# Performance work log

Measured on AMD Instinct MI355X. Metric: run time of the kernel, lower is better.

Reference implementation:

```python
import jax, jax.numpy as jnp
import numpy as np

N = 32768; NS = 16; C_MAIN = 128; C_MOD = 128; C_IN = 16; SHARE = 8
EPS = 1e-5; CHUNK = 1024
C_OUT = C_MAIN + C_MOD  # out_main = in_main + in_mod
C_W = C_IN // SHARE     # attention-weight channels = 2


def _bn(x, g, b, m, v):
    # BatchNorm1d in eval mode, per last-dim channel
    return (x - m) / jnp.sqrt(v + EPS) * g + b


def _knn(p, k):
    # exact kNN (self included, distance 0), chunked to bound memory
    def f(q):  # q: (CHUNK, 3)
        d = jnp.sum((q[:, None, :] - p[None, :, :]) ** 2, axis=-1)  # (CHUNK, N)
        return jax.lax.top_k(-d, k)[1]
    return jax.lax.map(f, p.reshape(-1, CHUNK, 3)).reshape(-1, k)


def setup_inputs() -> dict:
    key = jax.random.key(0)
    ks = iter(jax.random.split(key, 24))
    rn = lambda shape, s=0.1: jax.random.normal(next(ks), shape, jnp.float32) * s
    inp = {}
    inp["x_main"] = jax.random.normal(next(ks), (N, C_MAIN), jnp.float32)
    inp["x_mod"] = jax.random.normal(next(ks), (N, C_MOD), jnp.float32)
    inp["xyz"] = jax.random.uniform(next(ks), (N, 3), dtype=jnp.float32)
    inp["W_ein"] = rn((C_OUT, C_IN)); inp["b_ein"] = rn((C_IN,))
    inp["W_eout"] = rn((C_IN, C_OUT)); inp["b_eout"] = rn((C_OUT,))
    inp["Wq"] = rn((C_IN, C_IN)); inp["bq"] = rn((C_IN,))
    inp["Wk"] = rn((C_IN, C_IN)); inp["bk"] = rn((C_IN,))
    inp["Wv"] = rn((C_IN, C_IN)); inp["bv"] = rn((C_IN,))
    inp["Wp1"] = rn((3, 3)); inp["bp1"] = rn((3,))
    inp["Wp2"] = rn((3, C_IN)); inp["bp2"] = rn((C_IN,))
    inp["Wl1"] = rn((C_IN, C_W)); inp["bl1"] = rn((C_W,))
    inp["Wl2"] = rn((C_W, C_W)); inp["bl2"] = rn((C_W,))
    for name, c in (("bn_p", 3), ("bn_w1", C_IN), ("bn_w2", C_W)):
        inp[name + "_g"] = jnp.ones(c, jnp.float32)
        inp[name + "_b"] = jnp.zeros(c, jnp.float32)
        inp[name + "_m"] = jnp.zeros(c, jnp.float32)
        inp[name + "_v"] = jnp.ones(c, jnp.float32)
    return inp


def _forward(x_main, x_mod, xyz, W_ein, b_ein, W_eout, b_eout, Wq, bq, Wk, bk, Wv, bv,
             Wp1, bp1, Wp2, bp2, Wl1, bl1, Wl2, bl2,
             bn_p_g, bn_p_b, bn_p_m, bn_p_v,
             bn_w1_g, bn_w1_b, bn_w1_m, bn_w1_v,
             bn_w2_g, bn_w2_b, bn_w2_m, bn_w2_v, idx):
    x_fused = jnp.concatenate([x_main, x_mod], axis=-1)   # (N, 256)
    x_res = x_fused
    h = x_fused @ W_ein + b_ein                           # E_in: (N, 16)
    # PointTransformerLayer (local vector self-attention over NS neighbors)
    xq = h @ Wq + bq
    xk = h @ Wk + bk
    xv = h @ Wv + bv
    p_r = xyz[idx] - xyz[:, None, :]                      # relative coords (N, NS, 3)
    g_k = xk[idx]                                         # grouped keys   (N, NS, 16)
    g_v = xv[idx]                                         # grouped values (N, NS, 16)
    # linear_p: Linear(3,3) -> BN -> ReLU -> Linear(3, C_IN)
    t = jax.nn.relu(_bn(p_r @ Wp1 + bp1, bn_p_g, bn_p_b, bn_p_m, bn_p_v))
    p_e = t @ Wp2 + bp2                                   # (N, NS, 16)
    # out_planes//mid_planes == 1, so the .view(...).sum(2) on p_e is identity
    w = g_k - xq[:, None, :] + p_e
    # linear_w: BN -> ReLU -> Linear(16,2) -> BN -> ReLU -> Linear(2,2)
    w = jax.nn.relu(_bn(w, bn_w1_g, bn_w1_b, bn_w1_m, bn_w1_v))
    w = w @ Wl1 + bl1
    w = jax.nn.relu(_bn(w, bn_w2_g, bn_w2_b, bn_w2_m, bn_w2_v))
    w = w @ Wl2 + bl2                                     # (N, NS, 2)
    w = jax.nn.softmax(w, axis=1)                         # softmax over neighbors
    agg = ((g_v + p_e).reshape(N, NS, SHARE, C_W) * w[:, :, None, :]).sum(1).reshape(N, C_IN)
    return agg @ W_eout + b_eout + x_res                  # E_out + residual


def reference(x_main, x_mod, xyz, W_ein, b_ein, W_eout, b_eout, Wq, bq, Wk, bk, Wv, bv,
              Wp1, bp1, Wp2, bp2, Wl1, bl1, Wl2, bl2,
              bn_p_g, bn_p_b, bn_p_m, bn_p_v,
              bn_w1_g, bn_w1_b, bn_w1_m, bn_w1_v,
              bn_w2_g, bn_w2_b, bn_w2_m, bn_w2_v):
    idx = _knn(xyz, NS)
    return _forward(x_main, x_mod, xyz, W_ein, b_ein, W_eout, b_eout, Wq, bq, Wk, bk, Wv, bv,
                    Wp1, bp1, Wp2, bp2, Wl1, bl1, Wl2, bl2,
                    bn_p_g, bn_p_b, bn_p_m, bn_p_v,
                    bn_w1_g, bn_w1_b, bn_w1_m, bn_w1_v,
                    bn_w2_g, bn_w2_b, bn_w2_m, bn_w2_v, idx)
```

## Files before the change

### kernel.cpp

```cpp
#include <hip/hip_runtime.h>
#include <cstdint>

#define NPTS 32768
#define K 16
#define G 16
#define NCELL (G*G*G)

typedef unsigned short u16;
typedef unsigned int u32;

__device__ __forceinline__ float bf(u16 v) { return __uint_as_float(((u32)v) << 16); }
__device__ __forceinline__ void unp(u32 u, float& a, float& b) {
    a = __uint_as_float(u << 16);
    b = __uint_as_float(u & 0xffff0000u);
}
__device__ __forceinline__ u32 f2b(float f) {
    u32 x = __float_as_uint(f);
    return (x + 0x7fffu + ((x >> 16) & 1u)) >> 16;
}
__device__ __forceinline__ float ldw(const void* p, int j, bool isb) {
    return isb ? bf(((const u16*)p)[j]) : ((const float*)p)[j];
}
__device__ __forceinline__ void ld8(const void* p, size_t i, int cb, bool isb, float xs[8]) {
    if (isb) {
        const uint4* r = (const uint4*)((const u16*)p + i * 128);
        const uint4 u = r[cb];
        unp(u.x, xs[0], xs[1]); unp(u.y, xs[2], xs[3]);
        unp(u.z, xs[4], xs[5]); unp(u.w, xs[6], xs[7]);
    } else {
        const float4* r = (const float4*)((const float*)p + i * 128);
        const float4 a = r[2 * cb], b = r[2 * cb + 1];
        xs[0] = a.x; xs[1] = a.y; xs[2] = a.z; xs[3] = a.w;
        xs[4] = b.x; xs[5] = b.y; xs[6] = b.z; xs[7] = b.w;
    }
}
__device__ __forceinline__ int cellco(float x) {
    int c = (int)(x * (float)G);
    return c < 0 ? 0 : (c > G - 1 ? G - 1 : c);
}

__global__ __launch_bounds__(128) void k_feats(
    const void* __restrict__ xm, const void* __restrict__ xd, const void* __restrict__ xyz,
    const void* __restrict__ Wein, const void* __restrict__ bein,
    const void* __restrict__ Wq, const void* __restrict__ bq,
    const void* __restrict__ Wk, const void* __restrict__ bk,
    const void* __restrict__ Wv, const void* __restrict__ bv,
    const u32* __restrict__ sigp,
    float* __restrict__ oq, float* __restrict__ ok, float* __restrict__ ov,
    float4* __restrict__ xyzf, int* __restrict__ cellCnt)
{
    const bool isb = (*sigp == 0x3F803F80u);
    __shared__ float sW[4096];
    __shared__ float sM[768];
    __shared__ float sB[64];
    const int t = threadIdx.x;
    if (blockIdx.x < 32) cellCnt[blockIdx.x * 128 + t] = 0;
    for (int u = t; u < 4096; u += 128) sW[u] = ldw(Wein, u, isb);
    for (int u = t; u < 256; u += 128) {
        sM[u] = ldw(Wq, u, isb); sM[256 + u] = ldw(Wk, u, isb); sM[512 + u] = ldw(Wv, u, isb);
    }
    if (t < 64) {
        const void* bsrc = (t < 16) ? bein : (t < 32) ? bq : (t < 48) ? bk : bv;
        sB[t] = ldw(bsrc, t & 15, isb);
    }
    __syncthreads();
    const int i = blockIdx.x * 128 + t;
    float h[16];
#pragma unroll
    for (int j = 0; j < 16; ++j) h[j] = sB[j];
#pragma unroll 2
    for (int cb = 0; cb < 32; ++cb) {
        float xs[8];
        ld8((cb < 16) ? xm : xd, (size_t)i, cb & 15, isb, xs);
        const int c0 = cb * 8;
#pragma unroll
        for (int u = 0; u < 8; ++u) {
            const float x = xs[u];
            const float* w = &sW[(c0 + u) * 16];
#pragma unroll
            for (int j = 0; j < 16; ++j) h[j] = fmaf(x, w[j], h[j]);
        }
    }
    float* outs[3] = { oq, ok, ov };
#pragma unroll
    for (int m3 = 0; m3 < 3; ++m3) {
        float acc[16];
#pragma unroll
        for (int j = 0; j < 16; ++j) acc[j] = sB[16 + m3 * 16 + j];
        const float* wm = &sM[m3 * 256];
#pragma unroll
        for (int m = 0; m < 16; ++m) {
            const float hm = h[m];
#pragma unroll
            for (int j = 0; j < 16; ++j) acc[j] = fmaf(hm, wm[m * 16 + j], acc[j]);
        }
        float* o = outs[m3] + (size_t)i * 16;
#pragma unroll
        for (int j = 0; j < 16; ++j) o[j] = acc[j];
    }
    if (isb) {
        const u16* z = (const u16*)xyz;
        xyzf[i] = make_float4(bf(z[i * 3]), bf(z[i * 3 + 1]), bf(z[i * 3 + 2]), 0.f);
    } else {
        const float* z = (const float*)xyz;
        xyzf[i] = make_float4(z[i * 3], z[i * 3 + 1], z[i * 3 + 2], 0.f);
    }
}

__global__ __launch_bounds__(256) void k_cell(const float4* __restrict__ xyzf,
    int* __restrict__ cellCnt, int* __restrict__ ptCell, int* __restrict__ ptRank)
{
    const int i = blockIdx.x * 256 + threadIdx.x;
    const float4 p = xyzf[i];
    const int c = (cellco(p.z) * G + cellco(p.y)) * G + cellco(p.x);
    ptCell[i] = c;
    ptRank[i] = atomicAdd(&cellCnt[c], 1);
}

__global__ __launch_bounds__(1024) void k_scan(const int* __restrict__ cnt, int* __restrict__ starts)
{
    __shared__ int part[1024];
    const int t = threadIdx.x;
    const int c0 = cnt[4 * t], c1 = cnt[4 * t + 1], c2 = cnt[4 * t + 2], c3 = cnt[4 * t + 3];
    const int s = c0 + c1 + c2 + c3;
    part[t] = s;
    __syncthreads();
    for (int off = 1; off < 1024; off <<= 1) {
        const int u = (t >= off) ? part[t - off] : 0;
        __syncthreads();
        part[t] += u;
        __syncthreads();
    }
    const int excl = part[t] - s;
    starts[4 * t] = excl;
    starts[4 * t + 1] = excl + c0;
    starts[4 * t + 2] = excl + c0 + c1;
    starts[4 * t + 3] = excl + c0 + c1 + c2;
    if (t == 1023) starts[NCELL] = part[1023];
}

__global__ __launch_bounds__(256) void k_scatter(const float4* __restrict__ xyzf,
    const int* __restrict__ ptCell, const int* __restrict__ ptRank,
    const int* __restrict__ starts, float4* __restrict__ sorted)
{
    const int i = blockIdx.x * 256 + threadIdx.x;
    float4 p = xyzf[i];
    p.w = __int_as_float(i);
    sorted[starts[ptCell[i]] + ptRank[i]] = p;
}

__device__ __forceinline__ bool lexlt(float d1, int i1, float d2, int i2) {
    return (d1 < d2) || (d1 == d2 && i1 < i2);
}

__device__ __forceinline__ void insert16(float d, int ci, float bd[K], int bi[K]) {
    if (lexlt(d, ci, bd[K - 1], bi[K - 1])) {
        float cd = d;
#pragma unroll
        for (int j = 0; j < K; ++j) {
            const bool lt = lexlt(cd, ci, bd[j], bi[j]);
            const float td = lt ? bd[j] : cd;
            const int   ti = lt ? bi[j] : ci;
            bd[j] = lt ? cd : bd[j];
            bi[j] = lt ? ci : bi[j];
            cd = td; ci = ti;
        }
    }
}

__device__ __forceinline__ void scan_strided(const float4* __restrict__ sorted,
    int b, int e, int l, float qx, float qy, float qz, float bd[K], int bi[K])
{
    int p = b + l;
    if (p >= e) return;
    float4 c = sorted[p];
    while (true) {
        const int pn = p + 4;
        const bool more = pn < e;
        float4 cnx = c;
        if (more) cnx = sorted[pn];
        const float dx = __fsub_rn(qx, c.x);
        const float dy = __fsub_rn(qy, c.y);
        const float dz = __fsub_rn(qz, c.z);
        const float d = __fadd_rn(__fadd_rn(__fmul_rn(dx, dx), __fmul_rn(dy, dy)), __fmul_rn(dz, dz));
        insert16(d, __float_as_int(c.w), bd, bi);
        if (!more) break;
        c = cnx; p = pn;
    }
}

__device__ __forceinline__ void merge16(float d[K], int ii[K], int mask) {
    float pd[K]; int pi[K];
#pragma unroll
    for (int i = 0; i < K; ++i) {
        pd[i] = __shfl_xor(d[K - 1 - i], mask, 64);
        pi[i] = __shfl_xor(ii[K - 1 - i], mask, 64);
    }
#pragma unroll
    for (int i = 0; i < K; ++i) {
        const bool keep = lexlt(d[i], ii[i], pd[i], pi[i]);
        d[i] = keep ? d[i] : pd[i];
        ii[i] = keep ? ii[i] : pi[i];
    }
#pragma unroll
    for (int ks = 8; ks >= 1; ks >>= 1) {
#pragma unroll
        for (int i = 0; i < K; ++i) {
            if ((i & ks) == 0) {
                const int j = i + ks;
                const bool sw = lexlt(d[j], ii[j], d[i], ii[i]);
                const float t1 = d[i]; const int t2 = ii[i];
                d[i] = sw ? d[j] : d[i]; ii[i] = sw ? ii[j] : ii[i];
                d[j] = sw ? t1 : d[j];  ii[j] = sw ? t2 : ii[j];
            }
        }
    }
}

__device__ __forceinline__ float guard_radius(float qx, float qy, float qz,
                                              int cx, int cy, int cz, int R)
{
    const float h = 1.0f / (float)G;
    float rg = 3.4e38f;
    if (cx - R >= 1)     rg = fminf(rg, qx - (float)(cx - R) * h);
    if (cx + R <= G - 2) rg = fminf(rg, (float)(cx + R + 1) * h - qx);
    if (cy - R >= 1)     rg = fminf(rg, qy - (float)(cy - R) * h);
    if (cy + R <= G - 2) rg = fminf(rg, (float)(cy + R + 1) * h - qy);
    if (cz - R >= 1)     rg = fminf(rg, qz - (float)(cz - R) * h);
    if (cz + R <= G - 2) rg = fminf(rg, (float)(cz + R + 1) * h - qz);
    return rg;
}

__global__ __launch_bounds__(256) void k_knng(const float4* __restrict__ sorted,
    const int* __restrict__ starts, int* __restrict__ idxOut)
{
    const int g = blockIdx.x * 256 + threadIdx.x;
    const int s = g >> 2;
    const int l = g & 3;
    const float4 me = sorted[s];
    const int orig = __float_as_int(me.w);
    const int cx = cellco(me.x), cy = cellco(me.y), cz = cellco(me.z);
    float bd[K]; int bi[K];
#pragma unroll
    for (int j = 0; j < K; ++j) { bd[j] = 3.4e38f; bi[j] = 0x7fffffff; }

    int bArr[9], eArr[9];
#pragma unroll
    for (int r = 0; r < 9; ++r) {
        const int dz = r / 3 - 1, dy = r % 3 - 1;
        const int zz = cz + dz, yy = cy + dy;
        if ((unsigned)zz > (unsigned)(G - 1) || (unsigned)yy > (unsigned)(G - 1)) {
            bArr[r] = 0; eArr[r] = 0;
        } else {
            const int base = (zz * G + yy) * G;
            const int x0 = cx - 1 < 0 ? 0 : cx - 1;
            const int x1 = cx + 1 > G - 1 ? G - 1 : cx + 1;
            bArr[r] = starts[base + x0];
            eArr[r] = starts[base + x1 + 1];
        }
    }
#pragma unroll
    for (int r = 0; r < 9; ++r)
        scan_strided(sorted, bArr[r], eArr[r], l, me.x, me.y, me.z, bd, bi);

    int R = 1;
    float td[K]; int ti[K];
    while (true) {
#pragma unroll
        for (int j = 0; j < K; ++j) { td[j] = bd[j]; ti[j] = bi[j]; }
        merge16(td, ti, 1);
        merge16(td, ti, 2);
        const float rg = guard_radius(me.x, me.y, me.z, cx, cy, cz, R);
        if (td[K - 1] < rg * rg * 0.9999f || R >= G) break;
        ++R;
        for (int dz = -R; dz <= R; ++dz) {
            const int zz = cz + dz;
            if ((unsigned)zz > (unsigned)(G - 1)) continue;
            const int az = dz < 0 ? -dz : dz;
            for (int dy = -R; dy <= R; ++dy) {
                const int yy = cy + dy;
                if ((unsigned)yy > (unsigned)(G - 1)) continue;
                const int ay = dy < 0 ? -dy : dy;
                const int base = (zz * G + yy) * G;
                if (az == R || ay == R) {
                    const int x0 = cx - R < 0 ? 0 : cx - R;
                    const int x1 = cx + R > G - 1 ? G - 1 : cx + R;
                    scan_strided(sorted, starts[base + x0], starts[base + x1 + 1], l,
                                 me.x, me.y, me.z, bd, bi);
                } else {
                    if (cx - R >= 0)
                        scan_strided(sorted, starts[base + cx - R], starts[base + cx - R + 1], l,
                                     me.x, me.y, me.z, bd, bi);
                    if (cx + R <= G - 1)
                        scan_strided(sorted, starts[base + cx + R], starts[base + cx + R + 1], l,
                                     me.x, me.y, me.z, bd, bi);
                }
            }
        }
    }
    if (l == 0) {
        int4* o = (int4*)(idxOut + (size_t)orig * K);
#pragma unroll
        for (int j4 = 0; j4 < 4; ++j4)
            o[j4] = make_int4(ti[4 * j4], ti[4 * j4 + 1], ti[4 * j4 + 2], ti[4 * j4 + 3]);
    }
}

__global__ __launch_bounds__(256) void k_attn(
    const void* __restrict__ xm, const void* __restrict__ xd,
    const float4* __restrict__ xyzf,
    const float* __restrict__ xq, const float* __restrict__ xk, const float* __restrict__ xv,
    const int* __restrict__ idx,
    const void* __restrict__ Weout, const void* __restrict__ beout,
    const void* __restrict__ Wp1, const void* __restrict__ bp1,
    const void* __restrict__ Wp2, const void* __restrict__ bp2,
    const void* __restrict__ Wl1, const void* __restrict__ bl1,
    const void* __restrict__ Wl2, const void* __restrict__ bl2,
    const void* __restrict__ bnp_g, const void* __restrict__ bnp_b, const void* __restrict__ bnp_m, const void* __restrict__ bnp_v,
    const void* __restrict__ bw1_g, const void* __restrict__ bw1_b, const void* __restrict__ bw1_m, const void* __restrict__ bw1_v,
    const void* __restrict__ bw2_g, const void* __restrict__ bw2_b, const void* __restrict__ bw2_m, const void* __restrict__ bw2_v,
    void* __restrict__ out)
{
    const bool isb = (*(const u32*)bnp_g == 0x3F803F80u);
    __shared__ float sWe[4096];
    __shared__ float sbe[256];
    __shared__ float sWp2[48];
    __shared__ float sbp2[16];
    __shared__ float sWl1[32];
    __shared__ float s1[16], o1[16];
    const int t = threadIdx.x;
    for (int u = t; u < 4096; u += 256) sWe[u] = ldw(Weout, u, isb);
    if (t < 256) sbe[t] = ldw(beout, t, isb);
    if (t < 48) sWp2[t] = ldw(Wp2, t, isb);
    if (t < 16) sbp2[t] = ldw(bp2, t, isb);
    if (t < 32) sWl1[t] = ldw(Wl1, t, isb);
    if (t < 16) {
        const float s = ldw(bw1_g, t, isb) / sqrtf(ldw(bw1_v, t, isb) + 1e-5f);
        s1[t] = s; o1[t] = ldw(bw1_b, t, isb) - ldw(bw1_m, t, isb) * s;
    }
    __syncthreads();
    const int g = blockIdx.x * 256 + t;
    const int s = g >> 2;
    const int l = g & 3;
    float Wp1r[9], bp1r[3], sp[3], op[3];
#pragma unroll
    for (int u = 0; u < 9; ++u) Wp1r[u] = ldw(Wp1, u, isb);
#pragma unroll
    for (int a = 0; a < 3; ++a) {
        const float sc = ldw(bnp_g, a, isb) / sqrtf(ldw(bnp_v, a, isb) + 1e-5f);
        sp[a] = sc; op[a] = ldw(bnp_b, a, isb) - ldw(bnp_m, a, isb) * sc;
        bp1r[a] = ldw(bp1, a, isb);
    }
    float Wl2r[4], bl1r[2], bl2r[2], s2[2], o2[2];
#pragma unroll
    for (int u = 0; u < 4; ++u) Wl2r[u] = ldw(Wl2, u, isb);
#pragma unroll
    for (int c = 0; c < 2; ++c) {
        bl1r[c] = ldw(bl1, c, isb); bl2r[c] = ldw(bl2, c, isb);
        const float sc = ldw(bw2_g, c, isb) / sqrtf(ldw(bw2_v, c, isb) + 1e-5f);
        s2[c] = sc; o2[c] = ldw(bw2_b, c, isb) - ldw(bw2_m, c, isb) * sc;
    }
    float q[16];
    const float4* qrow = (const float4*)(xq + (size_t)s * 16);
#pragma unroll
    for (int j4 = 0; j4 < 4; ++j4) {
        const float4 v = qrow[j4];
        q[4 * j4] = v.x; q[4 * j4 + 1] = v.y; q[4 * j4 + 2] = v.z; q[4 * j4 + 3] = v.w;
    }
    const int4 nb4 = ((const int4*)(idx + (size_t)s * 16))[l];
    const int nb[4] = { nb4.x, nb4.y, nb4.z, nb4.w };
    const float4 cp = xyzf[s];
    float wa[4], wb[4], ttx[4], tty[4], ttz[4];
#pragma unroll
    for (int n = 0; n < 4; ++n) {
        const int nn = nb[n];
        const float4 pp = xyzf[nn];
        const float prx = pp.x - cp.x, pry = pp.y - cp.y, prz = pp.z - cp.z;
        float tt[3];
#pragma unroll
        for (int a = 0; a < 3; ++a) {
            float v = prx * Wp1r[a] + pry * Wp1r[3 + a] + prz * Wp1r[6 + a] + bp1r[a];
            v = fmaf(v, sp[a], op[a]);
            tt[a] = v > 0.f ? v : 0.f;
        }
        ttx[n] = tt[0]; tty[n] = tt[1]; ttz[n] = tt[2];
        const float* kk = &xk[(size_t)nn * 16];
        float wl0 = bl1r[0], wl1v = bl1r[1];
#pragma unroll
        for (int j = 0; j < 16; ++j) {
            const float pe = tt[0] * sWp2[j] + tt[1] * sWp2[16 + j] + tt[2] * sWp2[32 + j] + sbp2[j];
            float w = kk[j] - q[j] + pe;
            w = fmaf(w, s1[j], o1[j]); w = w > 0.f ? w : 0.f;
            wl0 = fmaf(w, sWl1[2 * j], wl0);
            wl1v = fmaf(w, sWl1[2 * j + 1], wl1v);
        }
        float y0 = fmaf(wl0, s2[0], o2[0]); y0 = y0 > 0.f ? y0 : 0.f;
        float y1 = fmaf(wl1v, s2[1], o2[1]); y1 = y1 > 0.f ? y1 : 0.f;
        wa[n] = y0 * Wl2r[0] + y1 * Wl2r[2] + bl2r[0];
        wb[n] = y0 * Wl2r[1] + y1 * Wl2r[3] + bl2r[1];
    }
    float m0 = fmaxf(fmaxf(wa[0], wa[1]), fmaxf(wa[2], wa[3]));
    float m1 = fmaxf(fmaxf(wb[0], wb[1]), fmaxf(wb[2], wb[3]));
    m0 = fmaxf(m0, __shfl_xor(m0, 1, 64)); m0 = fmaxf(m0, __shfl_xor(m0, 2, 64));
    m1 = fmaxf(m1, __shfl_xor(m1, 1, 64)); m1 = fmaxf(m1, __shfl_xor(m1, 2, 64));
    float sA = 0.f, sB = 0.f;
#pragma unroll
    for (int n = 0; n < 4; ++n) {
        wa[n] = __expf(wa[n] - m0); sA += wa[n];
        wb[n] = __expf(wb[n] - m1); sB += wb[n];
    }
    sA += __shfl_xor(sA, 1, 64); sA += __shfl_xor(sA, 2, 64);
    sB += __shfl_xor(sB, 1, 64); sB += __shfl_xor(sB, 2, 64);
    const float rA = 1.f / sA, rB = 1.f / sB;
    float agg[16];
#pragma unroll
    for (int j = 0; j < 16; ++j) agg[j] = 0.f;
#pragma unroll
    for (int n = 0; n < 4; ++n) {
        const float wA = wa[n] * rA, wB = wb[n] * rB;
        const float* vv = &xv[(size_t)nb[n] * 16];
#pragma unroll
        for (int j = 0; j < 16; ++j) {
            const float pe = ttx[n] * sWp2[j] + tty[n] * sWp2[16 + j] + ttz[n] * sWp2[32 + j] + sbp2[j];
            agg[j] = fmaf(vv[j] + pe, (j & 1) ? wB : wA, agg[j]);
        }
    }
#pragma unroll
    for (int j = 0; j < 16; ++j) {
        agg[j] += __shfl_xor(agg[j], 1, 64);
        agg[j] += __shfl_xor(agg[j], 2, 64);
    }
#pragma unroll 1
    for (int obi = 0; obi < 8; ++obi) {
        const int ob = obi * 4 + l;
        float xs[8];
        ld8((ob < 16) ? xm : xd, (size_t)s, ob & 15, isb, xs);
        const int o0 = ob * 8;
        float acc[8];
#pragma unroll
        for (int u = 0; u < 8; ++u) acc[u] = sbe[o0 + u] + xs[u];
#pragma unroll
        for (int j = 0; j < 16; ++j) {
            const float aj = agg[j];
            const float* w = &sWe[j * 256 + o0];
#pragma unroll
            for (int u = 0; u < 8; ++u) acc[u] = fmaf(aj, w[u], acc[u]);
        }
        if (isb) {
            u32* orow = (u32*)out + (size_t)s * 128;
#pragma unroll
            for (int u = 0; u < 4; ++u)
                orow[ob * 4 + u] = f2b(acc[2 * u]) | (f2b(acc[2 * u + 1]) << 16);
        } else {
            float4* orow = (float4*)((float*)out + (size_t)s * 256);
            orow[2 * ob]     = make_float4(acc[0], acc[1], acc[2], acc[3]);
            orow[2 * ob + 1] = make_float4(acc[4], acc[5], acc[6], acc[7]);
        }
    }
}

extern "C" void kernel_launch(void* const* d_in, const int* in_sizes, int n_in,
                              void* d_out, int out_size, void* d_ws, size_t ws_size,
                              hipStream_t stream)
{
    (void)in_sizes; (void)n_in; (void)out_size; (void)ws_size;
    const void* xm   = d_in[0];
    const void* xd   = d_in[1];
    const void* xyz  = d_in[2];
    const void* Wein = d_in[3];
    const void* bein = d_in[4];
    const void* Weout= d_in[5];
    const void* beout= d_in[6];
    const void* Wq   = d_in[7];
    const void* bq   = d_in[8];
    const void* Wk   = d_in[9];
    const void* bk   = d_in[10];
    const void* Wv   = d_in[11];
    const void* bv   = d_in[12];
    const void* Wp1  = d_in[13];
    const void* bp1  = d_in[14];
    const void* Wp2  = d_in[15];
    const void* bp2  = d_in[16];
    const void* Wl1  = d_in[17];
    const void* bl1  = d_in[18];
    const void* Wl2  = d_in[19];
    const void* bl2  = d_in[20];
    const void* bnp_g = d_in[21];
    const void* bnp_b = d_in[22];
    const void* bnp_m = d_in[23];
    const void* bnp_v = d_in[24];
    const void* bw1_g = d_in[25];
    const void* bw1_b = d_in[26];
    const void* bw1_m = d_in[27];
    const void* bw1_v = d_in[28];
    const void* bw2_g = d_in[29];
    const void* bw2_b = d_in[30];
    const void* bw2_m = d_in[31];
    const void* bw2_v = d_in[32];

    char* ws = (char*)d_ws;
    const size_t MB = 1024 * 1024;
    float*  oq    = (float*)(ws);
    float*  ok    = (float*)(ws + 2 * MB);
    float*  ov    = (float*)(ws + 4 * MB);
    int*    idx   = (int*)  (ws + 6 * MB);
    float4* xyzf  = (float4*)(ws + 8 * MB);
    float4* sortp = (float4*)(ws + 8 * MB + 512 * 1024);
    int* cellCnt  = (int*)(ws + 9 * MB);
    int* starts   = (int*)(ws + 9 * MB + 32 * 1024);
    int* ptCell   = (int*)(ws + 9 * MB + 64 * 1024);
    int* ptRank   = (int*)(ws + 9 * MB + 192 * 1024);

    k_feats<<<dim3(NPTS / 128), dim3(128), 0, stream>>>(
        xm, xd, xyz, Wein, bein, Wq, bq, Wk, bk, Wv, bv,
        (const u32*)bnp_g, oq, ok, ov, xyzf, cellCnt);
    k_cell<<<dim3(NPTS / 256), dim3(256), 0, stream>>>(xyzf, cellCnt, ptCell, ptRank);
    k_scan<<<dim3(1), dim3(1024), 0, stream>>>(cellCnt, starts);
    k_scatter<<<dim3(NPTS / 256), dim3(256), 0, stream>>>(xyzf, ptCell, ptRank, starts, sortp);
    k_knng<<<dim3(NPTS * 4 / 256), dim3(256), 0, stream>>>(sortp, starts, idx);
    k_attn<<<dim3(NPTS * 4 / 256), dim3(256), 0, stream>>>(
        xm, xd, xyzf, oq, ok, ov, idx, Weout, beout, Wp1, bp1, Wp2, bp2,
        Wl1, bl1, Wl2, bl2, bnp_g, bnp_b, bnp_m, bnp_v,
        bw1_g, bw1_b, bw1_m, bw1_v, bw2_g, bw2_b, bw2_m, bw2_v, d_out);
}
```

Measured before the change: 296.0 us.

## Pack kNN keys into u64, prune cells by bound, widen lanes per point

Several changes at once. The kNN search now keeps distance and index packed into one u64 key, so each comparison is a single integer compare. It skips neighbour cells whose minimum distance already exceeds the current shared 16th-best bound (tau8 across lanes), and uses 8 lanes per query instead of 4. The feature kernel splits each row's input projection across two threads and fuses in the cell-binning step. The attention kernel also uses 8 lanes per point with float4 gathers, and the scan uses wave shuffles. Together these aim to cut distance evaluations and raise parallelism, at the cost of extra shuffle traffic and code complexity.

```diff
diff --git a/kernel.cpp b/kernel.cpp
--- a/kernel.cpp
+++ b/kernel.cpp
@@ -8,6 +8,7 @@
 
 typedef unsigned short u16;
 typedef unsigned int u32;
+typedef unsigned long long u64;
 
 __device__ __forceinline__ float bf(u16 v) { return __uint_as_float(((u32)v) << 16); }
 __device__ __forceinline__ void unp(u32 u, float& a, float& b) {
@@ -38,8 +39,11 @@
     int c = (int)(x * (float)G);
     return c < 0 ? 0 : (c > G - 1 ? G - 1 : c);
 }
-
-__global__ __launch_bounds__(128) void k_feats(
+__device__ __forceinline__ u64 shflx64(u64 v, int m) {
+    return (u64)__shfl_xor((long long)v, m, 64);
+}
+
+__global__ __launch_bounds__(256) void k_feats(
     const void* __restrict__ xm, const void* __restrict__ xd, const void* __restrict__ xyz,
     const void* __restrict__ Wein, const void* __restrict__ bein,
     const void* __restrict__ Wq, const void* __restrict__ bq,
@@ -47,96 +51,104 @@
     const void* __restrict__ Wv, const void* __restrict__ bv,
     const u32* __restrict__ sigp,
     float* __restrict__ oq, float* __restrict__ ok, float* __restrict__ ov,
-    float4* __restrict__ xyzf, int* __restrict__ cellCnt)
+    float4* __restrict__ xyzf, int* __restrict__ cellCnt,
+    int* __restrict__ ptCell, int* __restrict__ ptRank)
 {
     const bool isb = (*sigp == 0x3F803F80u);
     __shared__ float sW[4096];
     __shared__ float sM[768];
     __shared__ float sB[64];
     const int t = threadIdx.x;
-    if (blockIdx.x < 32) cellCnt[blockIdx.x * 128 + t] = 0;
-    for (int u = t; u < 4096; u += 128) sW[u] = ldw(Wein, u, isb);
-    for (int u = t; u < 256; u += 128) {
-        sM[u] = ldw(Wq, u, isb); sM[256 + u] = ldw(Wk, u, isb); sM[512 + u] = ldw(Wv, u, isb);
-    }
+    for (int u = t; u < 4096; u += 256) sW[u] = ldw(Wein, u, isb);
+    if (t < 256) { sM[t] = ldw(Wq, t, isb); sM[256 + t] = ldw(Wk, t, isb); sM[512 + t] = ldw(Wv, t, isb); }
     if (t < 64) {
         const void* bsrc = (t < 16) ? bein : (t < 32) ? bq : (t < 48) ? bk : bv;
         sB[t] = ldw(bsrc, t & 15, isb);
     }
     __syncthreads();
-    const int i = blockIdx.x * 128 + t;
-    float h[16];
-#pragma unroll
-    for (int j = 0; j < 16; ++j) h[j] = sB[j];
+    const int r = blockIdx.x * 128 + (t >> 1);
+    const int half = t & 1;
+    float hp[16];
+#pragma unroll
+    for (int j = 0; j < 16; ++j) hp[j] = half ? 0.f : sB[j];
+    const void* src = half ? xd : xm;
+    const int wbase = half * 128;
 #pragma unroll 2
-    for (int cb = 0; cb < 32; ++cb) {
+    for (int cb = 0; cb < 16; ++cb) {
         float xs[8];
-        ld8((cb < 16) ? xm : xd, (size_t)i, cb & 15, isb, xs);
-        const int c0 = cb * 8;
+        ld8(src, (size_t)r, cb, isb, xs);
 #pragma unroll
         for (int u = 0; u < 8; ++u) {
             const float x = xs[u];
-            const float* w = &sW[(c0 + u) * 16];
-#pragma unroll
-            for (int j = 0; j < 16; ++j) h[j] = fmaf(x, w[j], h[j]);
-        }
-    }
-    float* outs[3] = { oq, ok, ov };
-#pragma unroll
-    for (int m3 = 0; m3 < 3; ++m3) {
-        float acc[16];
-#pragma unroll
-        for (int j = 0; j < 16; ++j) acc[j] = sB[16 + m3 * 16 + j];
-        const float* wm = &sM[m3 * 256];
-#pragma unroll
-        for (int m = 0; m < 16; ++m) {
-            const float hm = h[m];
-#pragma unroll
-            for (int j = 0; j < 16; ++j) acc[j] = fmaf(hm, wm[m * 16 + j], acc[j]);
-        }
-        float* o = outs[m3] + (size_t)i * 16;
-#pragma unroll
-        for (int j = 0; j < 16; ++j) o[j] = acc[j];
-    }
-    if (isb) {
-        const u16* z = (const u16*)xyz;
-        xyzf[i] = make_float4(bf(z[i * 3]), bf(z[i * 3 + 1]), bf(z[i * 3 + 2]), 0.f);
-    } else {
-        const float* z = (const float*)xyz;
-        xyzf[i] = make_float4(z[i * 3], z[i * 3 + 1], z[i * 3 + 2], 0.f);
-    }
-}
-
-__global__ __launch_bounds__(256) void k_cell(const float4* __restrict__ xyzf,
-    int* __restrict__ cellCnt, int* __restrict__ ptCell, int* __restrict__ ptRank)
-{
-    const int i = blockIdx.x * 256 + threadIdx.x;
-    const float4 p = xyzf[i];
-    const int c = (cellco(p.z) * G + cellco(p.y)) * G + cellco(p.x);
-    ptCell[i] = c;
-    ptRank[i] = atomicAdd(&cellCnt[c], 1);
+            const float* w = &sW[(wbase + cb * 8 + u) * 16];
+#pragma unroll
+            for (int j = 0; j < 16; ++j) hp[j] = fmaf(x, w[j], hp[j]);
+        }
+    }
+    float h[16];
+#pragma unroll
+    for (int j = 0; j < 16; ++j) h[j] = hp[j] + __shfl_xor(hp[j], 1, 64);
+    const float* wm = half ? &sM[256] : &sM[0];
+    const float* bm = half ? &sB[32] : &sB[16];
+    float acc[16];
+#pragma unroll
+    for (int j = 0; j < 16; ++j) acc[j] = bm[j];
+#pragma unroll
+    for (int m = 0; m < 16; ++m) {
+        const float hm = h[m];
+#pragma unroll
+        for (int j = 0; j < 16; ++j) acc[j] = fmaf(hm, wm[m * 16 + j], acc[j]);
+    }
+    float4* o4 = (float4*)((half ? ok : oq) + (size_t)r * 16);
+#pragma unroll
+    for (int j4 = 0; j4 < 4; ++j4)
+        o4[j4] = make_float4(acc[4 * j4], acc[4 * j4 + 1], acc[4 * j4 + 2], acc[4 * j4 + 3]);
+    float vacc[8];
+    const int vo = half * 8;
+#pragma unroll
+    for (int u = 0; u < 8; ++u) vacc[u] = sB[48 + vo + u];
+#pragma unroll
+    for (int m = 0; m < 16; ++m) {
+        const float hm = h[m];
+#pragma unroll
+        for (int u = 0; u < 8; ++u) vacc[u] = fmaf(hm, sM[512 + m * 16 + vo + u], vacc[u]);
+    }
+    float4* v4 = (float4*)(ov + (size_t)r * 16 + vo);
+    v4[0] = make_float4(vacc[0], vacc[1], vacc[2], vacc[3]);
+    v4[1] = make_float4(vacc[4], vacc[5], vacc[6], vacc[7]);
+    if (half == 0) {
+        float px, py, pz;
+        if (isb) { const u16* z = (const u16*)xyz; px = bf(z[r * 3]); py = bf(z[r * 3 + 1]); pz = bf(z[r * 3 + 2]); }
+        else { const float* z = (const float*)xyz; px = z[r * 3]; py = z[r * 3 + 1]; pz = z[r * 3 + 2]; }
+        xyzf[r] = make_float4(px, py, pz, 0.f);
+        const int c = (cellco(pz) * G + cellco(py)) * G + cellco(px);
+        ptCell[r] = c;
+        ptRank[r] = atomicAdd(&cellCnt[c], 1);
+    }
 }
 
 __global__ __launch_bounds__(1024) void k_scan(const int* __restrict__ cnt, int* __restrict__ starts)
 {
-    __shared__ int part[1024];
+    __shared__ int wtot[16];
     const int t = threadIdx.x;
-    const int c0 = cnt[4 * t], c1 = cnt[4 * t + 1], c2 = cnt[4 * t + 2], c3 = cnt[4 * t + 3];
-    const int s = c0 + c1 + c2 + c3;
-    part[t] = s;
+    const int4 c4 = ((const int4*)cnt)[t];
+    const int s = c4.x + c4.y + c4.z + c4.w;
+    int inc = s;
+#pragma unroll
+    for (int off = 1; off < 64; off <<= 1) {
+        const int v = __shfl_up(inc, off, 64);
+        if ((t & 63) >= off) inc += v;
+    }
+    if ((t & 63) == 63) wtot[t >> 6] = inc;
     __syncthreads();
-    for (int off = 1; off < 1024; off <<= 1) {
-        const int u = (t >= off) ? part[t - off] : 0;
-        __syncthreads();
-        part[t] += u;
-        __syncthreads();
-    }
-    const int excl = part[t] - s;
-    starts[4 * t] = excl;
-    starts[4 * t + 1] = excl + c0;
-    starts[4 * t + 2] = excl + c0 + c1;
-    starts[4 * t + 3] = excl + c0 + c1 + c2;
-    if (t == 1023) starts[NCELL] = part[1023];
+    const int wid = t >> 6;
+    int wpre = 0;
+    for (int w = 0; w < wid; ++w) wpre += wtot[w];
+    const int excl = wpre + inc - s;
+    int4 st;
+    st.x = excl; st.y = excl + c4.x; st.z = excl + c4.x + c4.y; st.w = excl + c4.x + c4.y + c4.z;
+    ((int4*)starts)[t] = st;
+    if (t == 1023) starts[NCELL] = excl + s;
 }
 
 __global__ __launch_bounds__(256) void k_scatter(const float4* __restrict__ xyzf,
@@ -149,33 +161,26 @@
     sorted[starts[ptCell[i]] + ptRank[i]] = p;
 }
 
-__device__ __forceinline__ bool lexlt(float d1, int i1, float d2, int i2) {
-    return (d1 < d2) || (d1 == d2 && i1 < i2);
-}
-
-__device__ __forceinline__ void insert16(float d, int ci, float bd[K], int bi[K]) {
-    if (lexlt(d, ci, bd[K - 1], bi[K - 1])) {
-        float cd = d;
+__device__ __forceinline__ void ins16(u64 kb, u64 key[K]) {
+    if (kb < key[K - 1]) {
 #pragma unroll
         for (int j = 0; j < K; ++j) {
-            const bool lt = lexlt(cd, ci, bd[j], bi[j]);
-            const float td = lt ? bd[j] : cd;
-            const int   ti = lt ? bi[j] : ci;
-            bd[j] = lt ? cd : bd[j];
-            bi[j] = lt ? ci : bi[j];
-            cd = td; ci = ti;
-        }
-    }
-}
-
-__device__ __forceinline__ void scan_strided(const float4* __restrict__ sorted,
-    int b, int e, int l, float qx, float qy, float qz, float bd[K], int bi[K])
+            const bool lt = kb < key[j];
+            const u64 tk = lt ? key[j] : kb;
+            key[j] = lt ? kb : key[j];
+            kb = tk;
+        }
+    }
+}
+
+__device__ __forceinline__ void scan_run8(const float4* __restrict__ sorted,
+    int b, int e, int l, float qx, float qy, float qz, u64 key[K])
 {
     int p = b + l;
     if (p >= e) return;
     float4 c = sorted[p];
     while (true) {
-        const int pn = p + 4;
+        const int pn = p + 8;
         const bool more = pn < e;
         float4 cnx = c;
         if (more) cnx = sorted[pn];
@@ -183,35 +188,37 @@
         const float dy = __fsub_rn(qy, c.y);
         const float dz = __fsub_rn(qz, c.z);
         const float d = __fadd_rn(__fadd_rn(__fmul_rn(dx, dx), __fmul_rn(dy, dy)), __fmul_rn(dz, dz));
-        insert16(d, __float_as_int(c.w), bd, bi);
+        ins16(((u64)__float_as_uint(d) << 32) | (u32)__float_as_int(c.w), key);
         if (!more) break;
         c = cnx; p = pn;
     }
 }
 
-__device__ __forceinline__ void merge16(float d[K], int ii[K], int mask) {
-    float pd[K]; int pi[K];
-#pragma unroll
-    for (int i = 0; i < K; ++i) {
-        pd[i] = __shfl_xor(d[K - 1 - i], mask, 64);
-        pi[i] = __shfl_xor(ii[K - 1 - i], mask, 64);
-    }
-#pragma unroll
-    for (int i = 0; i < K; ++i) {
-        const bool keep = lexlt(d[i], ii[i], pd[i], pi[i]);
-        d[i] = keep ? d[i] : pd[i];
-        ii[i] = keep ? ii[i] : pi[i];
-    }
+__device__ __forceinline__ u64 tau8(const u64 key[K]) {
+    u64 b1 = key[15], b2 = key[1];
+#pragma unroll
+    for (int m = 1; m <= 4; m <<= 1) {
+        const u64 o1 = shflx64(b1, m); b1 = o1 < b1 ? o1 : b1;
+        const u64 o2 = shflx64(b2, m); b2 = o2 > b2 ? o2 : b2;
+    }
+    return b1 < b2 ? b1 : b2;
+}
+
+__device__ __forceinline__ void merge16k(u64 k[K], int mask) {
+    u64 pk[K];
+#pragma unroll
+    for (int i = 0; i < K; ++i) pk[i] = shflx64(k[K - 1 - i], mask);
+#pragma unroll
+    for (int i = 0; i < K; ++i) k[i] = k[i] < pk[i] ? k[i] : pk[i];
 #pragma unroll
     for (int ks = 8; ks >= 1; ks >>= 1) {
 #pragma unroll
         for (int i = 0; i < K; ++i) {
             if ((i & ks) == 0) {
                 const int j = i + ks;
-                const bool sw = lexlt(d[j], ii[j], d[i], ii[i]);
-                const float t1 = d[i]; const int t2 = ii[i];
-                d[i] = sw ? d[j] : d[i]; ii[i] = sw ? ii[j] : ii[i];
-                d[j] = sw ? t1 : d[j];  ii[j] = sw ? t2 : ii[j];
+                const u64 a = k[i], b = k[j];
+                k[i] = a < b ? a : b;
+                k[j] = a < b ? b : a;
             }
         }
     }
@@ -235,74 +242,83 @@
     const int* __restrict__ starts, int* __restrict__ idxOut)
 {
     const int g = blockIdx.x * 256 + threadIdx.x;
-    const int s = g >> 2;
-    const int l = g & 3;
+    const int s = g >> 3;
+    const int l = g & 7;
     const float4 me = sorted[s];
     const int orig = __float_as_int(me.w);
     const int cx = cellco(me.x), cy = cellco(me.y), cz = cellco(me.z);
-    float bd[K]; int bi[K];
-#pragma unroll
-    for (int j = 0; j < K; ++j) { bd[j] = 3.4e38f; bi[j] = 0x7fffffff; }
-
-    int bArr[9], eArr[9];
+    const float h = 1.0f / (float)G;
+    u64 key[K];
+#pragma unroll
+    for (int j = 0; j < K; ++j) key[j] = ~0ull;
+    u64 tk = ~0ull;
+
+    const int ord_dy[9] = { 0, -1, 1,  0, 0, -1, -1,  1, 1 };
+    const int ord_dz[9] = { 0,  0, 0, -1, 1, -1,  1, -1, 1 };
 #pragma unroll
     for (int r = 0; r < 9; ++r) {
-        const int dz = r / 3 - 1, dy = r % 3 - 1;
-        const int zz = cz + dz, yy = cy + dy;
-        if ((unsigned)zz > (unsigned)(G - 1) || (unsigned)yy > (unsigned)(G - 1)) {
-            bArr[r] = 0; eArr[r] = 0;
-        } else {
-            const int base = (zz * G + yy) * G;
-            const int x0 = cx - 1 < 0 ? 0 : cx - 1;
-            const int x1 = cx + 1 > G - 1 ? G - 1 : cx + 1;
-            bArr[r] = starts[base + x0];
-            eArr[r] = starts[base + x1 + 1];
-        }
-    }
-#pragma unroll
-    for (int r = 0; r < 9; ++r)
-        scan_strided(sorted, bArr[r], eArr[r], l, me.x, me.y, me.z, bd, bi);
-
+        const int dy = ord_dy[r], dz = ord_dz[r];
+        const int yy = cy + dy, zz = cz + dz;
+        if ((unsigned)yy > (unsigned)(G - 1) || (unsigned)zz > (unsigned)(G - 1)) continue;
+        const float dyd = dy < 0 ? me.y - (float)cy * h : dy > 0 ? (float)(cy + 1) * h - me.y : 0.f;
+        const float dzd = dz < 0 ? me.z - (float)cz * h : dz > 0 ? (float)(cz + 1) * h - me.z : 0.f;
+        const u64 mk = (u64)__float_as_uint((dyd * dyd + dzd * dzd) * 0.9999f) << 32;
+        if (tk < mk) continue;
+        const int base = (zz * G + yy) * G;
+        const int x0 = cx - 1 < 0 ? 0 : cx - 1;
+        const int x1 = cx + 1 > G - 1 ? G - 1 : cx + 1;
+        scan_run8(sorted, starts[base + x0], starts[base + x1 + 1], l, me.x, me.y, me.z, key);
+        tk = tau8(key);
+    }
     int R = 1;
-    float td[K]; int ti[K];
-    while (true) {
-#pragma unroll
-        for (int j = 0; j < K; ++j) { td[j] = bd[j]; ti[j] = bi[j]; }
-        merge16(td, ti, 1);
-        merge16(td, ti, 2);
+    while (R < G) {
         const float rg = guard_radius(me.x, me.y, me.z, cx, cy, cz, R);
-        if (td[K - 1] < rg * rg * 0.9999f || R >= G) break;
+        if (tk < ((u64)__float_as_uint(rg * rg * 0.9999f) << 32)) break;
         ++R;
         for (int dz = -R; dz <= R; ++dz) {
             const int zz = cz + dz;
             if ((unsigned)zz > (unsigned)(G - 1)) continue;
             const int az = dz < 0 ? -dz : dz;
+            const float dzd = dz < 0 ? me.z - (float)(cz + dz + 1) * h : dz > 0 ? (float)(cz + dz) * h - me.z : 0.f;
             for (int dy = -R; dy <= R; ++dy) {
                 const int yy = cy + dy;
                 if ((unsigned)yy > (unsigned)(G - 1)) continue;
                 const int ay = dy < 0 ? -dy : dy;
+                const float dyd = dy < 0 ? me.y - (float)(cy + dy + 1) * h : dy > 0 ? (float)(cy + dy) * h - me.y : 0.f;
+                const float myz = dzd * dzd + dyd * dyd;
                 const int base = (zz * G + yy) * G;
                 if (az == R || ay == R) {
+                    if (tk < ((u64)__float_as_uint(myz * 0.9999f) << 32)) continue;
                     const int x0 = cx - R < 0 ? 0 : cx - R;
                     const int x1 = cx + R > G - 1 ? G - 1 : cx + R;
-                    scan_strided(sorted, starts[base + x0], starts[base + x1 + 1], l,
-                                 me.x, me.y, me.z, bd, bi);
+                    scan_run8(sorted, starts[base + x0], starts[base + x1 + 1], l, me.x, me.y, me.z, key);
+                    tk = tau8(key);
                 } else {
-                    if (cx - R >= 0)
-                        scan_strided(sorted, starts[base + cx - R], starts[base + cx - R + 1], l,
-                                     me.x, me.y, me.z, bd, bi);
-                    if (cx + R <= G - 1)
-                        scan_strided(sorted, starts[base + cx + R], starts[base + cx + R + 1], l,
-                                     me.x, me.y, me.z, bd, bi);
+                    if (cx - R >= 0) {
+                        const float xd = me.x - (float)(cx - R + 1) * h;
+                        if (!(tk < ((u64)__float_as_uint((myz + xd * xd) * 0.9999f) << 32))) {
+                            scan_run8(sorted, starts[base + cx - R], starts[base + cx - R + 1], l, me.x, me.y, me.z, key);
+                            tk = tau8(key);
+                        }
+                    }
+                    if (cx + R <= G - 1) {
+                        const float xd = (float)(cx + R) * h - me.x;
+                        if (!(tk < ((u64)__float_as_uint((myz + xd * xd) * 0.9999f) << 32))) {
+                            scan_run8(sorted, starts[base + cx + R], starts[base + cx + R + 1], l, me.x, me.y, me.z, key);
+                            tk = tau8(key);
+                        }
+                    }
                 }
             }
         }
     }
+    merge16k(key, 1); merge16k(key, 2); merge16k(key, 4);
     if (l == 0) {
         int4* o = (int4*)(idxOut + (size_t)orig * K);
 #pragma unroll
         for (int j4 = 0; j4 < 4; ++j4)
-            o[j4] = make_int4(ti[4 * j4], ti[4 * j4 + 1], ti[4 * j4 + 2], ti[4 * j4 + 3]);
+            o[j4] = make_int4((int)(u32)key[4 * j4], (int)(u32)key[4 * j4 + 1],
+                              (int)(u32)key[4 * j4 + 2], (int)(u32)key[4 * j4 + 3]);
     }
 }
 
@@ -340,8 +356,8 @@
     }
     __syncthreads();
     const int g = blockIdx.x * 256 + t;
-    const int s = g >> 2;
-    const int l = g & 3;
+    const int s = g >> 3;
+    const int l = g & 7;
     float Wp1r[9], bp1r[3], sp[3], op[3];
 #pragma unroll
     for (int u = 0; u < 9; ++u) Wp1r[u] = ldw(Wp1, u, isb);
@@ -367,12 +383,12 @@
         const float4 v = qrow[j4];
         q[4 * j4] = v.x; q[4 * j4 + 1] = v.y; q[4 * j4 + 2] = v.z; q[4 * j4 + 3] = v.w;
     }
-    const int4 nb4 = ((const int4*)(idx + (size_t)s * 16))[l];
-    const int nb[4] = { nb4.x, nb4.y, nb4.z, nb4.w };
+    const int2 nb2 = ((const int2*)(idx + (size_t)s * 16))[l];
+    const int nb[2] = { nb2.x, nb2.y };
     const float4 cp = xyzf[s];
-    float wa[4], wb[4], ttx[4], tty[4], ttz[4];
-#pragma unroll
-    for (int n = 0; n < 4; ++n) {
+    float wa[2], wb[2], ttx[2], tty[2], ttz[2];
+#pragma unroll
+    for (int n = 0; n < 2; ++n) {
         const int nn = nb[n];
         const float4 pp = xyzf[nn];
         const float prx = pp.x - cp.x, pry = pp.y - cp.y, prz = pp.z - cp.z;
@@ -384,7 +400,13 @@
             tt[a] = v > 0.f ? v : 0.f;
         }
         ttx[n] = tt[0]; tty[n] = tt[1]; ttz[n] = tt[2];
-        const float* kk = &xk[(size_t)nn * 16];
+        const float4* k4 = (const float4*)(xk + (size_t)nn * 16);
+        float kk[16];
+#pragma unroll
+        for (int j4 = 0; j4 < 4; ++j4) {
+            const float4 v = k4[j4];
+            kk[4 * j4] = v.x; kk[4 * j4 + 1] = v.y; kk[4 * j4 + 2] = v.z; kk[4 * j4 + 3] = v.w;
+        }
         float wl0 = bl1r[0], wl1v = bl1r[1];
 #pragma unroll
         for (int j = 0; j < 16; ++j) {
@@ -399,26 +421,37 @@
         wa[n] = y0 * Wl2r[0] + y1 * Wl2r[2] + bl2r[0];
         wb[n] = y0 * Wl2r[1] + y1 * Wl2r[3] + bl2r[1];
     }
-    float m0 = fmaxf(fmaxf(wa[0], wa[1]), fmaxf(wa[2], wa[3]));
-    float m1 = fmaxf(fmaxf(wb[0], wb[1]), fmaxf(wb[2], wb[3]));
-    m0 = fmaxf(m0, __shfl_xor(m0, 1, 64)); m0 = fmaxf(m0, __shfl_xor(m0, 2, 64));
-    m1 = fmaxf(m1, __shfl_xor(m1, 1, 64)); m1 = fmaxf(m1, __shfl_xor(m1, 2, 64));
+    float m0 = fmaxf(wa[0], wa[1]), m1 = fmaxf(wb[0], wb[1]);
+#pragma unroll
+    for (int m = 1; m <= 4; m <<= 1) {
+        m0 = fmaxf(m0, __shfl_xor(m0, m, 64));
+        m1 = fmaxf(m1, __shfl_xor(m1, m, 64));
+    }
     float sA = 0.f, sB = 0.f;
 #pragma unroll
-    for (int n = 0; n < 4; ++n) {
+    for (int n = 0; n < 2; ++n) {
         wa[n] = __expf(wa[n] - m0); sA += wa[n];
         wb[n] = __expf(wb[n] - m1); sB += wb[n];
     }
-    sA += __shfl_xor(sA, 1, 64); sA += __shfl_xor(sA, 2, 64);
-    sB += __shfl_xor(sB, 1, 64); sB += __shfl_xor(sB, 2, 64);
+#pragma unroll
+    for (int m = 1; m <= 4; m <<= 1) {
+        sA += __shfl_xor(sA, m, 64);
+        sB += __shfl_xor(sB, m, 64);
+    }
     const float rA = 1.f / sA, rB = 1.f / sB;
     float agg[16];
 #pragma unroll
     for (int j = 0; j < 16; ++j) agg[j] = 0.f;
 #pragma unroll
-    for (int n = 0; n < 4; ++n) {
+    for (int n = 0; n < 2; ++n) {
         const float wA = wa[n] * rA, wB = wb[n] * rB;
-        const float* vv = &xv[(size_t)nb[n] * 16];
+        const float4* v4 = (const float4*)(xv + (size_t)nb[n] * 16);
+        float vv[16];
+#pragma unroll
+        for (int j4 = 0; j4 < 4; ++j4) {
+            const float4 v = v4[j4];
+            vv[4 * j4] = v.x; vv[4 * j4 + 1] = v.y; vv[4 * j4 + 2] = v.z; vv[4 * j4 + 3] = v.w;
+        }
 #pragma unroll
         for (int j = 0; j < 16; ++j) {
             const float pe = ttx[n] * sWp2[j] + tty[n] * sWp2[16 + j] + ttz[n] * sWp2[32 + j] + sbp2[j];
@@ -429,10 +462,11 @@
     for (int j = 0; j < 16; ++j) {
         agg[j] += __shfl_xor(agg[j], 1, 64);
         agg[j] += __shfl_xor(agg[j], 2, 64);
+        agg[j] += __shfl_xor(agg[j], 4, 64);
     }
 #pragma unroll 1
-    for (int obi = 0; obi < 8; ++obi) {
-        const int ob = obi * 4 + l;
+    for (int obi = 0; obi < 4; ++obi) {
+        const int ob = obi * 8 + l;
         float xs[8];
         ld8((ob < 16) ? xm : xd, (size_t)s, ob & 15, isb, xs);
         const int o0 = ob * 8;
@@ -511,14 +545,14 @@
     int* ptCell   = (int*)(ws + 9 * MB + 64 * 1024);
     int* ptRank   = (int*)(ws + 9 * MB + 192 * 1024);
 
-    k_feats<<<dim3(NPTS / 128), dim3(128), 0, stream>>>(
+    hipMemsetAsync(cellCnt, 0, NCELL * sizeof(int), stream);
+    k_feats<<<dim3(NPTS * 2 / 256), dim3(256), 0, stream>>>(
         xm, xd, xyz, Wein, bein, Wq, bq, Wk, bk, Wv, bv,
-        (const u32*)bnp_g, oq, ok, ov, xyzf, cellCnt);
-    k_cell<<<dim3(NPTS / 256), dim3(256), 0, stream>>>(xyzf, cellCnt, ptCell, ptRank);
+        (const u32*)bnp_g, oq, ok, ov, xyzf, cellCnt, ptCell, ptRank);
     k_scan<<<dim3(1), dim3(1024), 0, stream>>>(cellCnt, starts);
     k_scatter<<<dim3(NPTS / 256), dim3(256), 0, stream>>>(xyzf, ptCell, ptRank, starts, sortp);
-    k_knng<<<dim3(NPTS * 4 / 256), dim3(256), 0, stream>>>(sortp, starts, idx);
-    k_attn<<<dim3(NPTS * 4 / 256), dim3(256), 0, stream>>>(
+    k_knng<<<dim3(NPTS * 8 / 256), dim3(256), 0, stream>>>(sortp, starts, idx);
+    k_attn<<<dim3(NPTS * 8 / 256), dim3(256), 0, stream>>>(
         xm, xd, xyzf, oq, ok, ov, idx, Weout, beout, Wp1, bp1, Wp2, bp2,
         Wl1, bl1, Wl2, bl2, bnp_g, bnp_b, bnp_m, bnp_v,
         bw1_g, bw1_b, bw1_m, bw1_v, bw2_g, bw2_b, bw2_m, bw2_v, d_out);
```

Measured after the change: 268.2 us. 1.1x faster.
